# Kernel optimization log

Hardware: AMD Instinct MI355X
Metric: run time of the kernel (lower is better)

Reference implementation:

```python
import jax, jax.numpy as jnp
import numpy as np

NUM_HEADS = 8
CHUNK = 64


def setup_inputs() -> dict:
    key = jax.random.key(0)
    k1, k2, k3, k4 = jax.random.split(key, 4)
    B, C, H, W = 16, 384, 64, 64
    x = jax.random.normal(k1, (B, C, H, W), dtype=jnp.float32)
    # torch nn.Linear weights are [out, in]; qkv has no bias (qkv_bias=False)
    qkv_w = jax.random.normal(k2, (3 * C, C), dtype=jnp.float32) * (C ** -0.5)
    proj_w = jax.random.normal(k3, (C, C), dtype=jnp.float32) * (C ** -0.5)
    proj_b = jax.random.normal(k4, (C,), dtype=jnp.float32) * 0.02
    return {"x": x, "qkv_w": qkv_w, "proj_w": proj_w, "proj_b": proj_b}


def reference(x, qkv_w, proj_w, proj_b):
    B, C, H, W = x.shape
    N = H * W
    nh = NUM_HEADS
    hd = C // nh
    scale = hd ** -0.5
    nc = N // CHUNK  # number of non-overlapping local blocks

    t = x.reshape(B, C, N).transpose(0, 2, 1)  # [B, N, C]
    qkv = t @ qkv_w.T  # [B, N, 3C]
    qkv = qkv.reshape(B, N, 3, nh, hd).transpose(2, 0, 3, 1, 4)  # [3, B, nh, N, hd]
    q, k, v = qkv[0], qkv[1], qkv[2]

    # block-local attention: reshape N -> (nc, CHUNK) and batch over blocks
    q = q.reshape(B, nh, nc, CHUNK, hd)
    k = k.reshape(B, nh, nc, CHUNK, hd)
    v = v.reshape(B, nh, nc, CHUNK, hd)

    scores = jnp.einsum('bhnqd,bhnkd->bhnqk', q, k) * scale  # [B,nh,nc,CHUNK,CHUNK]
    attn = jax.nn.softmax(scores, axis=-1)
    out = jnp.einsum('bhnqk,bhnkd->bhnqd', attn, v)  # [B,nh,nc,CHUNK,hd]

    out = out.reshape(B, nh, N, hd).transpose(0, 2, 1, 3).reshape(B, N, C)
    out = out @ proj_w.T + proj_b
    return out.transpose(0, 2, 1).reshape(B, C, H, W)
```

## Files before the change

### kernel.cpp

```cpp
#include <hip/hip_runtime.h>
#include <stdint.h>

#define NH 8
#define HD 48
#define CC 384
#define NN 4096
#define CK 384

typedef short short8 __attribute__((ext_vector_type(8)));
typedef float floatx4 __attribute__((ext_vector_type(4)));

__device__ inline unsigned short f32_to_bf16_bits(float f) {
    uint32_t u = __builtin_bit_cast(uint32_t, f);
    u = (u + 0x7FFFu + ((u >> 16) & 1u)) >> 16;
    return (unsigned short)u;
}
__device__ inline short8 load8(const unsigned short* p) {
    return *reinterpret_cast<const short8*>(p);
}
typedef __attribute__((address_space(1))) const void gvoid_t;
typedef __attribute__((address_space(3))) void lvoid_t;
__device__ inline void async16(const unsigned short* g, unsigned short* l) {
    __builtin_amdgcn_global_load_lds((gvoid_t*)g, (lvoid_t*)l, 16, 0, 0);
}

__global__ __launch_bounds__(256) void k_cvt(
    const float* __restrict__ src, unsigned short* __restrict__ dst, int n8)
{
    int i = blockIdx.x * 256 + threadIdx.x;
    if (i >= n8) return;
    const float* s = src + (size_t)i * 8;
    unsigned short t[8];
    #pragma unroll
    for (int j = 0; j < 8; ++j) t[j] = f32_to_bf16_bits(s[j]);
    *reinterpret_cast<short8*>(dst + (size_t)i * 8) = *reinterpret_cast<short8*>(t);
}

__global__ __launch_bounds__(256) void k_tr(
    const float* __restrict__ x, unsigned short* __restrict__ xT)
{
    __shared__ unsigned short tile[64][72];
    int bx = blockIdx.x;
    int nt = bx & 63; int rest = bx >> 6; int ct = rest % 6; int b = rest / 6;
    int c0 = ct * 64, n0 = nt * 64;
    int t = threadIdx.x;
    int nl = t & 63, w = t >> 6;
    const float* xb = x + (size_t)b * CC * NN;
    #pragma unroll
    for (int i = 0; i < 4; ++i) {
        int cl = w * 16 + i * 4;
        unsigned short u[4];
        #pragma unroll
        for (int j = 0; j < 4; ++j)
            u[j] = f32_to_bf16_bits(xb[(size_t)(c0 + cl + j) * NN + n0 + nl]);
        *reinterpret_cast<uint2*>(&tile[nl][cl]) = *reinterpret_cast<uint2*>(u);
    }
    __syncthreads();
    #pragma unroll
    for (int it = 0; it < 2; ++it) {
        int v = it * 256 + t;
        int row = v >> 3, seg = v & 7;
        *reinterpret_cast<short8*>(xT + ((size_t)b * NN + n0 + row) * CK + c0 + seg * 8) =
            load8(&tile[row][seg * 8]);
    }
}

__global__ __launch_bounds__(256) void k_qkv(
    const unsigned short* __restrict__ A,
    const unsigned short* __restrict__ W,
    unsigned short* __restrict__ QK,
    unsigned short* __restrict__ Vt)
{
    __shared__ unsigned short smem[24576];
    int bx = blockIdx.x;
    int l  = (bx & 7) * 576 + (bx >> 3);
    int tf = l % 9, tm = l / 9;
    int m0 = tm * 128, f0 = tf * 128;
    int tid = threadIdx.x, wid = tid >> 6, lane = tid & 63;
    int l15 = lane & 15, quad = lane >> 4;
    int wm = wid & 1, wn = wid >> 1;

    const unsigned short* Ab = A + (size_t)m0 * CK;
    const unsigned short* Wb = W + (size_t)f0 * CK;

    floatx4 acc[4][4] = {};

    auto stage = [&](int kt, int buf) {
        int k0 = kt * 32;
        unsigned short* Asd = smem + buf * 8192;
        unsigned short* Wsd = Asd + 4096;
        #pragma unroll
        for (int i = 0; i < 2; ++i) {
            int c = i * 256 + tid;
            int row = c >> 2;
            int sg  = (c & 3) ^ (row & 3);
            async16(Ab + (size_t)row * CK + k0 + sg * 8, Asd + (i * 256 + wid * 64) * 8);
            async16(Wb + (size_t)row * CK + k0 + sg * 8, Wsd + (i * 256 + wid * 64) * 8);
        }
    };
    int sx = (quad ^ (l15 & 3)) * 8;
    auto compute = [&](int buf) {
        unsigned short* As = smem + buf * 8192;
        unsigned short* Ws = As + 4096;
        short8 a[4], bf[4];
        #pragma unroll
        for (int i = 0; i < 4; ++i)
            a[i] = load8(As + (wm * 64 + i * 16 + l15) * 32 + sx);
        #pragma unroll
        for (int j = 0; j < 4; ++j)
            bf[j] = load8(Ws + (wn * 64 + j * 16 + l15) * 32 + sx);
        asm volatile("s_waitcnt lgkmcnt(0)" ::: "memory");
        __builtin_amdgcn_sched_barrier(0);
        #pragma unroll
        for (int i = 0; i < 4; ++i)
            #pragma unroll
            for (int j = 0; j < 4; ++j)
                acc[i][j] = __builtin_amdgcn_mfma_f32_16x16x32_bf16(a[i], bf[j], acc[i][j], 0, 0, 0);
    };

    stage(0, 0);
    stage(1, 1);
    asm volatile("s_waitcnt vmcnt(4)" ::: "memory");
    __builtin_amdgcn_sched_barrier(0);
    __builtin_amdgcn_s_barrier();
    __builtin_amdgcn_sched_barrier(0);

    int cur = 0;
    for (int kk = 0; kk < 10; ++kk) {
        int nb3 = cur + 2; if (nb3 >= 3) nb3 -= 3;
        stage(kk + 2, nb3);
        compute(cur);
        asm volatile("s_waitcnt vmcnt(4)" ::: "memory");
        __builtin_amdgcn_sched_barrier(0);
        __builtin_amdgcn_s_barrier();
        __builtin_amdgcn_sched_barrier(0);
        cur = cur + 1 == 3 ? 0 : cur + 1;
    }
    compute(cur);
    asm volatile("s_waitcnt vmcnt(0)" ::: "memory");
    __builtin_amdgcn_sched_barrier(0);
    __builtin_amdgcn_s_barrier();
    __builtin_amdgcn_sched_barrier(0);
    cur = cur + 1 == 3 ? 0 : cur + 1;
    compute(cur);
    __syncthreads();

    int b = m0 >> 12, nb = m0 & 4095;
    if (tf < 6) {
        #pragma unroll
        for (int i = 0; i < 4; ++i)
            #pragma unroll
            for (int j = 0; j < 4; ++j)
                #pragma unroll
                for (int r = 0; r < 4; ++r)
                    smem[(wm * 64 + i * 16 + quad * 4 + r) * 128 + wn * 64 + j * 16 + l15] =
                        f32_to_bf16_bits(acc[i][j][r]);
        __syncthreads();
        #pragma unroll
        for (int it = 0; it < 8; ++it) {
            int c = it * 256 + tid;
            int row = c >> 4, seg = c & 15;
            *reinterpret_cast<short8*>(QK + (size_t)(m0 + row) * 768 + f0 + seg * 8) =
                load8(smem + row * 128 + seg * 8);
        }
    } else {
        #pragma unroll
        for (int i = 0; i < 4; ++i)
            #pragma unroll
            for (int j = 0; j < 4; ++j)
                #pragma unroll
                for (int r = 0; r < 4; ++r)
                    smem[(wn * 64 + j * 16 + l15) * 136 + wm * 64 + i * 16 + quad * 4 + r] =
                        f32_to_bf16_bits(acc[i][j][r]);
        __syncthreads();
        int fvb = (tf - 6) * 128;
        #pragma unroll
        for (int it = 0; it < 8; ++it) {
            int c = it * 256 + tid;
            int fl = c >> 4, seg = c & 15;
            int fv = fvb + fl;
            int h = fv / 48, d = fv - h * 48;
            *reinterpret_cast<short8*>(Vt + (((size_t)(b * 8 + h) * 48 + d) << 12) + nb + seg * 8) =
                load8(smem + fl * 136 + seg * 8);
        }
    }
}

__global__ __launch_bounds__(256) void k_attn(
    const unsigned short* __restrict__ QK,
    const unsigned short* __restrict__ Vt,
    unsigned short* __restrict__ AO)
{
    __shared__ unsigned short ql[64][72];
    __shared__ unsigned short kl[64][72];
    __shared__ unsigned short vt[48][72];
    __shared__ float          sc[64][66];
    __shared__ unsigned short pl[64][72];

    int bx = blockIdx.x;
    int cn = bx & 63, h = (bx >> 6) & 7, b = bx >> 9;
    int n0 = cn * 64;
    int tid = threadIdx.x, wid = tid >> 6, lane = tid & 63;
    int l15 = lane & 15, quad = lane >> 4;
    int m0w = wid * 16;
    int h48 = h * 48;
    size_t b4 = (size_t)b * NN + n0;

    for (int v = tid; v < 768; v += 256) {
        int mat = v / 384;
        int idx = v - mat * 384;
        int rr = idx / 6, seg = idx - rr * 6;
        uint4 val = *reinterpret_cast<const uint4*>(QK + (b4 + rr) * 768 + mat * 384 + h48 + seg * 8);
        unsigned short* dst = mat ? &kl[rr][seg * 8] : &ql[rr][seg * 8];
        *reinterpret_cast<uint4*>(dst) = val;
    }
    {
        short8 z = {};
        int v = tid;
        if (v < 256) {
            int mat = v >> 7, rr = (v >> 1) & 63, half = v & 1;
            unsigned short* dst = mat ? &kl[rr][48 + half * 8] : &ql[rr][48 + half * 8];
            *reinterpret_cast<short8*>(dst) = z;
        }
    }
    for (int v = tid; v < 384; v += 256) {
        int d = v >> 3, seg = v & 7;
        *reinterpret_cast<uint4*>(&vt[d][seg * 8]) =
            *reinterpret_cast<const uint4*>(Vt + (((size_t)(b * 8 + h) * 48 + d) << 12) + n0 + seg * 8);
    }
    __syncthreads();

    const float scale = 0.14433756729740643f;
    #pragma unroll
    for (int t = 0; t < 4; ++t) {
        floatx4 sacc = {};
        #pragma unroll
        for (int ks = 0; ks < 2; ++ks) {
            short8 a  = load8(&ql[m0w + l15][ks * 32 + quad * 8]);
            short8 bb = load8(&kl[t * 16 + l15][ks * 32 + quad * 8]);
            sacc = __builtin_amdgcn_mfma_f32_16x16x32_bf16(a, bb, sacc, 0, 0, 0);
        }
        #pragma unroll
        for (int r = 0; r < 4; ++r)
            sc[m0w + quad * 4 + r][t * 16 + l15] = sacc[r] * scale;
    }
    __syncthreads();

    {
        int row = m0w + l15;
        int jb  = quad * 16;
        float ev[16];
        #pragma unroll
        for (int jj = 0; jj < 16; ++jj) ev[jj] = sc[row][jb + jj];
        float m = ev[0];
        #pragma unroll
        for (int jj = 1; jj < 16; ++jj) m = fmaxf(m, ev[jj]);
        m = fmaxf(m, __shfl_xor(m, 16));
        m = fmaxf(m, __shfl_xor(m, 32));
        float s = 0.f;
        #pragma unroll
        for (int jj = 0; jj < 16; ++jj) { ev[jj] = __expf(ev[jj] - m); s += ev[jj]; }
        s += __shfl_xor(s, 16);
        s += __shfl_xor(s, 32);
        float inv = 1.0f / s;
        #pragma unroll
        for (int jj = 0; jj < 16; ++jj) pl[row][jb + jj] = f32_to_bf16_bits(ev[jj] * inv);
    }
    __syncthreads();

    #pragma unroll
    for (int t = 0; t < 3; ++t) {
        floatx4 oacc = {};
        #pragma unroll
        for (int ks = 0; ks < 2; ++ks) {
            short8 a  = load8(&pl[m0w + l15][ks * 32 + quad * 8]);
            short8 bb = load8(&vt[t * 16 + l15][ks * 32 + quad * 8]);
            oacc = __builtin_amdgcn_mfma_f32_16x16x32_bf16(a, bb, oacc, 0, 0, 0);
        }
        #pragma unroll
        for (int r = 0; r < 4; ++r)
            kl[m0w + quad * 4 + r][t * 16 + l15] = f32_to_bf16_bits(oacc[r]);
    }
    __syncthreads();

    for (int v = tid; v < 384; v += 256) {
        int rr = v / 6, seg = v - rr * 6;
        *reinterpret_cast<short8*>(AO + (b4 + rr) * CC + h48 + seg * 8) =
            load8(&kl[rr][seg * 8]);
    }
}

__global__ __launch_bounds__(256) void k_proj(
    const unsigned short* __restrict__ A,
    const unsigned short* __restrict__ W,
    const float* __restrict__ bias,
    float* __restrict__ out)
{
    __shared__ unsigned short smem[24576];
    float* fs = (float*)smem;
    int bx = blockIdx.x;
    int l  = (bx & 7) * 192 + (bx >> 3);
    int tf = l % 3, tm = l / 3;
    int m0 = tm * 128, f0 = tf * 128;
    int tid = threadIdx.x, wid = tid >> 6, lane = tid & 63;
    int l15 = lane & 15, quad = lane >> 4;
    int wm = wid & 1, wn = wid >> 1;

    const unsigned short* Ab = A + (size_t)m0 * CK;
    const unsigned short* Wb = W + (size_t)f0 * CK;

    floatx4 acc[4][4] = {};

    auto stage = [&](int kt, int buf) {
        int k0 = kt * 32;
        unsigned short* Asd = smem + buf * 8192;
        unsigned short* Wsd = Asd + 4096;
        #pragma unroll
        for (int i = 0; i < 2; ++i) {
            int c = i * 256 + tid;
            int row = c >> 2;
            int sg  = (c & 3) ^ (row & 3);
            async16(Ab + (size_t)row * CK + k0 + sg * 8, Asd + (i * 256 + wid * 64) * 8);
            async16(Wb + (size_t)row * CK + k0 + sg * 8, Wsd + (i * 256 + wid * 64) * 8);
        }
    };
    int sx = (quad ^ (l15 & 3)) * 8;
    auto compute = [&](int buf) {
        unsigned short* As = smem + buf * 8192;
        unsigned short* Ws = As + 4096;
        short8 a[4], bf[4];
        #pragma unroll
        for (int i = 0; i < 4; ++i)
            a[i] = load8(As + (wm * 64 + i * 16 + l15) * 32 + sx);
        #pragma unroll
        for (int j = 0; j < 4; ++j)
            bf[j] = load8(Ws + (wn * 64 + j * 16 + l15) * 32 + sx);
        asm volatile("s_waitcnt lgkmcnt(0)" ::: "memory");
        __builtin_amdgcn_sched_barrier(0);
        #pragma unroll
        for (int i = 0; i < 4; ++i)
            #pragma unroll
            for (int j = 0; j < 4; ++j)
                acc[i][j] = __builtin_amdgcn_mfma_f32_16x16x32_bf16(a[i], bf[j], acc[i][j], 0, 0, 0);
    };

    stage(0, 0);
    stage(1, 1);
    asm volatile("s_waitcnt vmcnt(4)" ::: "memory");
    __builtin_amdgcn_sched_barrier(0);
    __builtin_amdgcn_s_barrier();
    __builtin_amdgcn_sched_barrier(0);

    int cur = 0;
    for (int kk = 0; kk < 10; ++kk) {
        int nb3 = cur + 2; if (nb3 >= 3) nb3 -= 3;
        stage(kk + 2, nb3);
        compute(cur);
        asm volatile("s_waitcnt vmcnt(4)" ::: "memory");
        __builtin_amdgcn_sched_barrier(0);
        __builtin_amdgcn_s_barrier();
        __builtin_amdgcn_sched_barrier(0);
        cur = cur + 1 == 3 ? 0 : cur + 1;
    }
    compute(cur);
    asm volatile("s_waitcnt vmcnt(0)" ::: "memory");
    __builtin_amdgcn_sched_barrier(0);
    __builtin_amdgcn_s_barrier();
    __builtin_amdgcn_sched_barrier(0);
    cur = cur + 1 == 3 ? 0 : cur + 1;
    compute(cur);
    __syncthreads();

    int b = m0 >> 12, nb = m0 & 4095;
    #pragma unroll
    for (int hh = 0; hh < 2; ++hh) {
        if (wn == hh) {
            #pragma unroll
            for (int j = 0; j < 4; ++j) {
                float bv = bias[f0 + hh * 64 + j * 16 + l15];
                #pragma unroll
                for (int i = 0; i < 4; ++i)
                    #pragma unroll
                    for (int r = 0; r < 4; ++r)
                        fs[(j * 16 + l15) * 132 + wm * 64 + i * 16 + quad * 4 + r] =
                            acc[i][j][r] + bv;
            }
        }
        __syncthreads();
        #pragma unroll
        for (int it = 0; it < 8; ++it) {
            int c = it * 256 + tid;
            int cl = c >> 5, seg = c & 31;
            *reinterpret_cast<float4*>(
                out + (((size_t)(b * CC + f0 + hh * 64 + cl)) << 12) + nb + seg * 4) =
                *reinterpret_cast<const float4*>(fs + cl * 132 + seg * 4);
        }
        __syncthreads();
    }
}

extern "C" void kernel_launch(void* const* d_in, const int* in_sizes, int n_in,
                              void* d_out, int out_size, void* d_ws, size_t ws_size,
                              hipStream_t stream) {
    const float* x      = (const float*)d_in[0];
    const float* qkv_w  = (const float*)d_in[1];
    const float* proj_w = (const float*)d_in[2];
    const float* proj_b = (const float*)d_in[3];
    float* out = (float*)d_out;

    const size_t nX  = (size_t)16 * CC * NN;
    const size_t nW1 = (size_t)3 * CC * CC;
    const size_t nW2 = (size_t)CC * CC;

    unsigned short* xT  = (unsigned short*)d_ws;
    unsigned short* w1b = xT  + nX;
    unsigned short* w2b = w1b + nW1;
    unsigned short* QK  = w2b + nW2;
    unsigned short* Vt  = QK  + (size_t)16 * NN * 768;
    unsigned short* AO  = Vt  + (size_t)16 * 8 * 48 * NN;

    k_tr  <<<dim3(16 * 6 * 64), dim3(256), 0, stream>>>(x, xT);
    k_cvt <<<dim3((int)(nW1 / 8 + 255) / 256), dim3(256), 0, stream>>>(qkv_w, w1b, (int)(nW1 / 8));
    k_cvt <<<dim3((int)(nW2 / 8 + 255) / 256), dim3(256), 0, stream>>>(proj_w, w2b, (int)(nW2 / 8));

    k_qkv <<<dim3(512 * 9), dim3(256), 0, stream>>>(xT, w1b, QK, Vt);
    k_attn<<<dim3(16 * 8 * 64), dim3(256), 0, stream>>>(QK, Vt, AO);
    k_proj<<<dim3(512 * 3), dim3(256), 0, stream>>>(AO, w2b, proj_b, out);
}
```

Baseline: 349.3 us.

## Fuse x transpose and bf16 conversion into QKV GEMM; merge weight casts

Removes the separate transpose/convert kernel by having the QKV GEMM load fp32 x directly, convert to bf16 in registers, and write transposed tiles to LDS with a register-staged double buffer. The two weight-conversion launches are merged into one kernel. This drops the xT intermediate write/read and two launches, but the GEMM now reads twice as many bytes of x per tile and replaces the three-stage async pipeline with a simpler synchronous one.

```diff
diff --git a/kernel.cpp b/kernel.cpp
--- a/kernel.cpp
+++ b/kernel.cpp
@@ -24,54 +24,27 @@
     __builtin_amdgcn_global_load_lds((gvoid_t*)g, (lvoid_t*)l, 16, 0, 0);
 }
 
-__global__ __launch_bounds__(256) void k_cvt(
-    const float* __restrict__ src, unsigned short* __restrict__ dst, int n8)
+__global__ __launch_bounds__(256) void k_cvt2(
+    const float* __restrict__ src1, int n1,
+    const float* __restrict__ src2, int n2,
+    unsigned short* __restrict__ dst)
 {
     int i = blockIdx.x * 256 + threadIdx.x;
-    if (i >= n8) return;
-    const float* s = src + (size_t)i * 8;
+    if (i >= n1 + n2) return;
+    const float* s = (i < n1) ? (src1 + (size_t)i * 8) : (src2 + (size_t)(i - n1) * 8);
     unsigned short t[8];
     #pragma unroll
     for (int j = 0; j < 8; ++j) t[j] = f32_to_bf16_bits(s[j]);
     *reinterpret_cast<short8*>(dst + (size_t)i * 8) = *reinterpret_cast<short8*>(t);
 }
 
-__global__ __launch_bounds__(256) void k_tr(
-    const float* __restrict__ x, unsigned short* __restrict__ xT)
-{
-    __shared__ unsigned short tile[64][72];
-    int bx = blockIdx.x;
-    int nt = bx & 63; int rest = bx >> 6; int ct = rest % 6; int b = rest / 6;
-    int c0 = ct * 64, n0 = nt * 64;
-    int t = threadIdx.x;
-    int nl = t & 63, w = t >> 6;
-    const float* xb = x + (size_t)b * CC * NN;
-    #pragma unroll
-    for (int i = 0; i < 4; ++i) {
-        int cl = w * 16 + i * 4;
-        unsigned short u[4];
-        #pragma unroll
-        for (int j = 0; j < 4; ++j)
-            u[j] = f32_to_bf16_bits(xb[(size_t)(c0 + cl + j) * NN + n0 + nl]);
-        *reinterpret_cast<uint2*>(&tile[nl][cl]) = *reinterpret_cast<uint2*>(u);
-    }
-    __syncthreads();
-    #pragma unroll
-    for (int it = 0; it < 2; ++it) {
-        int v = it * 256 + t;
-        int row = v >> 3, seg = v & 7;
-        *reinterpret_cast<short8*>(xT + ((size_t)b * NN + n0 + row) * CK + c0 + seg * 8) =
-            load8(&tile[row][seg * 8]);
-    }
-}
-
 __global__ __launch_bounds__(256) void k_qkv(
-    const unsigned short* __restrict__ A,
+    const float* __restrict__ x,
     const unsigned short* __restrict__ W,
     unsigned short* __restrict__ QK,
     unsigned short* __restrict__ Vt)
 {
-    __shared__ unsigned short smem[24576];
+    __shared__ unsigned short smem[26624];
     int bx = blockIdx.x;
     int l  = (bx & 7) * 576 + (bx >> 3);
     int tf = l % 9, tm = l / 9;
@@ -80,72 +53,92 @@
     int l15 = lane & 15, quad = lane >> 4;
     int wm = wid & 1, wn = wid >> 1;
 
-    const unsigned short* Ab = A + (size_t)m0 * CK;
+    int b = m0 >> 12, nb = m0 & 4095;
+    const float* xb = x + (size_t)b * CC * NN + nb;
     const unsigned short* Wb = W + (size_t)f0 * CK;
 
+    int c4  = tid >> 4;
+    int t4a = tid & 15;
+
     floatx4 acc[4][4] = {};
-
-    auto stage = [&](int kt, int buf) {
-        int k0 = kt * 32;
-        unsigned short* Asd = smem + buf * 8192;
-        unsigned short* Wsd = Asd + 4096;
-        #pragma unroll
-        for (int i = 0; i < 2; ++i) {
+    float xr[2][4][4];
+
+    auto xload = [&](int kt) {
+        int k0 = kt * 64;
+        #pragma unroll
+        for (int p = 0; p < 2; ++p) {
+            int tok4 = t4a + 16 * p;
+            #pragma unroll
+            for (int j = 0; j < 4; ++j) {
+                float4 v = *reinterpret_cast<const float4*>(
+                    xb + (size_t)(k0 + c4 * 4 + j) * NN + tok4 * 4);
+                const float* f = (const float*)&v;
+                #pragma unroll
+                for (int i = 0; i < 4; ++i) xr[p][j][i] = f[i];
+            }
+        }
+    };
+    auto xwrite = [&](int buf) {
+        unsigned short* As = smem + buf * 9216;
+        #pragma unroll
+        for (int p = 0; p < 2; ++p) {
+            int tok4 = t4a + 16 * p;
+            #pragma unroll
+            for (int i = 0; i < 4; ++i) {
+                unsigned short u[4];
+                #pragma unroll
+                for (int j = 0; j < 4; ++j) u[j] = f32_to_bf16_bits(xr[p][j][i]);
+                *reinterpret_cast<uint2*>(As + (tok4 * 4 + i) * 72 + c4 * 4) =
+                    *reinterpret_cast<uint2*>(u);
+            }
+        }
+    };
+    auto wstage = [&](int kt) {
+        int k0 = kt * 64;
+        unsigned short* Ws = smem + 18432;
+        #pragma unroll
+        for (int i = 0; i < 4; ++i) {
             int c = i * 256 + tid;
-            int row = c >> 2;
-            int sg  = (c & 3) ^ (row & 3);
-            async16(Ab + (size_t)row * CK + k0 + sg * 8, Asd + (i * 256 + wid * 64) * 8);
-            async16(Wb + (size_t)row * CK + k0 + sg * 8, Wsd + (i * 256 + wid * 64) * 8);
-        }
-    };
-    int sx = (quad ^ (l15 & 3)) * 8;
+            async16(Wb + (size_t)(c >> 3) * CK + k0 + (c & 7) * 8, Ws + (i * 256 + wid * 64) * 8);
+        }
+    };
     auto compute = [&](int buf) {
-        unsigned short* As = smem + buf * 8192;
-        unsigned short* Ws = As + 4096;
-        short8 a[4], bf[4];
-        #pragma unroll
-        for (int i = 0; i < 4; ++i)
-            a[i] = load8(As + (wm * 64 + i * 16 + l15) * 32 + sx);
-        #pragma unroll
-        for (int j = 0; j < 4; ++j)
-            bf[j] = load8(Ws + (wn * 64 + j * 16 + l15) * 32 + sx);
-        asm volatile("s_waitcnt lgkmcnt(0)" ::: "memory");
-        __builtin_amdgcn_sched_barrier(0);
-        #pragma unroll
-        for (int i = 0; i < 4; ++i)
+        unsigned short* As = smem + buf * 9216;
+        unsigned short* Ws = smem + 18432;
+        #pragma unroll
+        for (int ks = 0; ks < 2; ++ks) {
+            short8 a[4], bf[4];
+            #pragma unroll
+            for (int i = 0; i < 4; ++i)
+                a[i] = load8(As + (wm * 64 + i * 16 + l15) * 72 + ks * 32 + quad * 8);
             #pragma unroll
             for (int j = 0; j < 4; ++j)
-                acc[i][j] = __builtin_amdgcn_mfma_f32_16x16x32_bf16(a[i], bf[j], acc[i][j], 0, 0, 0);
-    };
-
-    stage(0, 0);
-    stage(1, 1);
-    asm volatile("s_waitcnt vmcnt(4)" ::: "memory");
-    __builtin_amdgcn_sched_barrier(0);
-    __builtin_amdgcn_s_barrier();
-    __builtin_amdgcn_sched_barrier(0);
+                bf[j] = load8(Ws + (wn * 64 + j * 16 + l15) * 64 + ks * 32 + quad * 8);
+            #pragma unroll
+            for (int i = 0; i < 4; ++i)
+                #pragma unroll
+                for (int j = 0; j < 4; ++j)
+                    acc[i][j] = __builtin_amdgcn_mfma_f32_16x16x32_bf16(a[i], bf[j], acc[i][j], 0, 0, 0);
+        }
+    };
+
+    xload(0);
+    wstage(0);
+    xwrite(0);
+    __syncthreads();
 
     int cur = 0;
-    for (int kk = 0; kk < 10; ++kk) {
-        int nb3 = cur + 2; if (nb3 >= 3) nb3 -= 3;
-        stage(kk + 2, nb3);
+    #pragma unroll
+    for (int kk = 0; kk < 6; ++kk) {
+        if (kk < 5) xload(kk + 1);
         compute(cur);
-        asm volatile("s_waitcnt vmcnt(4)" ::: "memory");
-        __builtin_amdgcn_sched_barrier(0);
-        __builtin_amdgcn_s_barrier();
-        __builtin_amdgcn_sched_barrier(0);
-        cur = cur + 1 == 3 ? 0 : cur + 1;
-    }
-    compute(cur);
-    asm volatile("s_waitcnt vmcnt(0)" ::: "memory");
-    __builtin_amdgcn_sched_barrier(0);
-    __builtin_amdgcn_s_barrier();
-    __builtin_amdgcn_sched_barrier(0);
-    cur = cur + 1 == 3 ? 0 : cur + 1;
-    compute(cur);
-    __syncthreads();
-
-    int b = m0 >> 12, nb = m0 & 4095;
+        if (kk < 5) xwrite(cur ^ 1);
+        __syncthreads();
+        if (kk < 5) wstage(kk + 1);
+        __syncthreads();
+        cur ^= 1;
+    }
+
     if (tf < 6) {
         #pragma unroll
         for (int i = 0; i < 4; ++i)
@@ -412,18 +405,17 @@
     const size_t nW1 = (size_t)3 * CC * CC;
     const size_t nW2 = (size_t)CC * CC;
 
-    unsigned short* xT  = (unsigned short*)d_ws;
-    unsigned short* w1b = xT  + nX;
-    unsigned short* w2b = w1b + nW1;
-    unsigned short* QK  = w2b + nW2;
+    unsigned short* xT  = (unsigned short*)d_ws; (void)xT;
+    unsigned short* w1b = (unsigned short*)d_ws + nX;
+    unsigned short* QK  = w1b + nW1 + nW2;
     unsigned short* Vt  = QK  + (size_t)16 * NN * 768;
     unsigned short* AO  = Vt  + (size_t)16 * 8 * 48 * NN;
-
-    k_tr  <<<dim3(16 * 6 * 64), dim3(256), 0, stream>>>(x, xT);
-    k_cvt <<<dim3((int)(nW1 / 8 + 255) / 256), dim3(256), 0, stream>>>(qkv_w, w1b, (int)(nW1 / 8));
-    k_cvt <<<dim3((int)(nW2 / 8 + 255) / 256), dim3(256), 0, stream>>>(proj_w, w2b, (int)(nW2 / 8));
-
-    k_qkv <<<dim3(512 * 9), dim3(256), 0, stream>>>(xT, w1b, QK, Vt);
+    unsigned short* w2b = w1b + nW1;
+
+    k_cvt2<<<dim3((int)((nW1 + nW2) / 8 + 255) / 256, 1, 1), dim3(256), 0, stream>>>(
+        qkv_w, (int)(nW1 / 8), proj_w, (int)(nW2 / 8), w1b);
+
+    k_qkv <<<dim3(512 * 9), dim3(256), 0, stream>>>(x, w1b, QK, Vt);
     k_attn<<<dim3(16 * 8 * 64), dim3(256), 0, stream>>>(QK, Vt, AO);
     k_proj<<<dim3(512 * 3), dim3(256), 0, stream>>>(AO, w2b, proj_b, out);
 }
```

Measured after the change: 410.7 us. 17.6% more time.
